# Kernel optimization log

Measured on AMD Instinct MI355X. Metric: run time of the kernel, lower is better.

Reference implementation:

```python
import jax, jax.numpy as jnp
import numpy as np

B, T, Z, AE, H, M, A = 32, 512, 128, 16, 1024, 5, 18
OUT = Z * 3 * M + 1  # 1921
K = M * Z  # per-component split size for logmix/mu/logstd


def setup_inputs() -> dict:
    key = jax.random.key(0)
    ks = jax.random.split(key, 9)
    s = 0.02
    return {
        "z": jax.random.normal(ks[0], (B, T, Z), jnp.float32),
        "actions": jax.random.randint(ks[1], (B, T), 0, A, jnp.int32),
        "dones": jax.random.randint(ks[2], (B, T), 0, 2, jnp.int32),
        "embed": jax.random.normal(ks[3], (A, AE), jnp.float32) * s,
        "W_ih": jax.random.normal(ks[4], (4 * H, Z + AE), jnp.float32) * s,
        "W_hh": jax.random.normal(ks[5], (4 * H, H), jnp.float32) * s,
        "b_ih": jnp.zeros((4 * H,), jnp.float32),
        "b_hh": jnp.zeros((4 * H,), jnp.float32),
        "W_out": jax.random.normal(ks[6], (OUT, H), jnp.float32) * s,
        "b_out": jnp.zeros((OUT,), jnp.float32),
    }


def reference(z, actions, dones, embed, W_ih, W_hh, b_ih, b_hh, W_out, b_out):
    a_emb = embed[actions]                              # [B,T,AE]
    inp = jnp.concatenate([z, a_emb], axis=2)           # [B,T,Z+AE]
    d = dones.astype(inp.dtype)                         # [B,T]
    # precompute input contribution to gates for all timesteps (one big GEMM)
    x_pre = jnp.einsum('btf,gf->btg', inp, W_ih) + b_ih + b_hh  # [B,T,4H]

    def cell(carry, xt):
        h, c = carry
        xg, dt = xt                                     # xg: [B,4H], dt: [B]
        gates = xg + h @ W_hh.T
        i, f, g, o = jnp.split(gates, 4, axis=1)        # torch LSTMCell order i,f,g,o
        c_new = jax.nn.sigmoid(f) * c + jax.nn.sigmoid(i) * jnp.tanh(g)
        h_new = jax.nn.sigmoid(o) * jnp.tanh(c_new)
        mask = (1.0 - dt)[:, None]                      # done-masking AFTER output
        return (h_new * mask, c_new * mask), h_new

    h0 = jnp.zeros((B, H), inp.dtype)
    _, hs = jax.lax.scan(cell, (h0, h0), (x_pre.transpose(1, 0, 2), d.T))
    hs = hs.transpose(1, 0, 2)[:, :-1]                  # [B,T-1,H]
    out = hs @ W_out.T + b_out                          # [B,T-1,OUT]

    logmix = out[..., :K].reshape(-1, M)
    mu = out[..., K:2 * K].reshape(-1, M)
    logstd = out[..., 2 * K:3 * K].reshape(-1, M)
    done_p = out[..., 3 * K:].squeeze(-1)               # [B,T-1]
    logmix = logmix - jax.scipy.special.logsumexp(logmix, axis=1, keepdims=True)
    return logmix, mu, logstd, done_p
```

## Files before the change

kernel.cpp:

```cpp
#include <hip/hip_runtime.h>
#include <hip/hip_bf16.h>


typedef float f4 __attribute__((ext_vector_type(4)));
typedef short s8 __attribute__((ext_vector_type(8)));
typedef unsigned short us8v __attribute__((ext_vector_type(8)));
typedef unsigned short us4v __attribute__((ext_vector_type(4)));
typedef unsigned long long u64;
typedef unsigned u32;

#define DEV __device__ __forceinline__

DEV unsigned short f2b(float f) {
  unsigned u = __float_as_uint(f);
  return (unsigned short)((u + 0x7FFFu + ((u >> 16) & 1u)) >> 16);
}
DEV float b2f(unsigned short s) { return __uint_as_float(((unsigned)s) << 16); }

DEV f4 MFMA(s8 a, s8 b, f4 c) {
  return __builtin_amdgcn_mfma_f32_16x16x32_bf16(a, b, c, 0, 0, 0);
}
DEV s8 LD8(const unsigned short* p) { return *reinterpret_cast<const s8*>(p); }

DEV u32 AL32(const u32* p) {
  return __hip_atomic_load(p, __ATOMIC_RELAXED, __HIP_MEMORY_SCOPE_AGENT);
}
DEV void AS(u64* p, u64 v) {
  __hip_atomic_store(p, v, __ATOMIC_RELAXED, __HIP_MEMORY_SCOPE_AGENT);
}

DEV float sigf(float x) {
  float e = __builtin_amdgcn_exp2f(x * -1.44269504f);
  return __builtin_amdgcn_rcpf(1.f + e);
}
DEV float tanhf_fast(float x) {
  float e = __builtin_amdgcn_exp2f(x * 2.88539008f);
  return 1.f - 2.f * __builtin_amdgcn_rcpf(e + 1.f);
}

static constexpr size_t WS_GCNT = 0;
static constexpr size_t WS_NACT = 2048;
static constexpr size_t WS_HDR  = 4096;
static constexpr size_t WS_META = 4352;
static constexpr size_t WS_LOFF = 69888;
static constexpr size_t WS_TMP  = 131072;
static constexpr size_t WS_ZT   = 131072;
static constexpr size_t WS_WOUT = 4325376;
static constexpr size_t WS_HS2  = 8261632;
static constexpr size_t WS_END  = 41816064;
static constexpr size_t DO_CALL = 35651584;

__global__ void cvt_wout_k(const float* __restrict__ W, unsigned short* __restrict__ o) {
  int i = blockIdx.x * 256 + threadIdx.x;
  if (i < 491776) {
    const float4 v = reinterpret_cast<const float4*>(W)[i];
    us4v u; u[0] = f2b(v.x); u[1] = f2b(v.y); u[2] = f2b(v.z); u[3] = f2b(v.w);
    reinterpret_cast<us4v*>(o)[i] = u;
  }
}

__global__ void cvt_z_k(const float* __restrict__ z, unsigned short* __restrict__ zt) {
  int i = blockIdx.x * 256 + threadIdx.x;
  if (i < 524288) {
    const float4 v = reinterpret_cast<const float4*>(z)[i];
    us4v u; u[0] = f2b(v.x); u[1] = f2b(v.y); u[2] = f2b(v.z); u[3] = f2b(v.w);
    reinterpret_cast<us4v*>(zt)[i] = u;
  }
}

__global__ void zero_hs_tail_k(u64* __restrict__ hs2) {
  int i = blockIdx.x * 256 + threadIdx.x;
  if (i < 8192) {
    int region = i >> 5, r = 16352 + (i & 31);
    hs2[(size_t)region * 16384 + r] = 0ull;
  }
}

__global__ __launch_bounds__(256) void seg_build_k(
    const int* __restrict__ dones, u32* __restrict__ tmp,
    u32* __restrict__ meta, u32* __restrict__ nact, u32* __restrict__ hdr,
    u32* __restrict__ loff) {
  __shared__ u32 hist[512];
  __shared__ u32 cur[512];
  __shared__ u32 scnt[32];
  const int tid = threadIdx.x;
  for (int i = tid; i < 512; i += 256) hist[i] = 0;
  __syncthreads();
  if (tid < 32) {
    int b = tid, cnt = 0, t0 = 0;
    for (int t = 1; t <= 511; ++t) {
      bool brk = (t == 511) || (dones[b * 512 + t - 1] != 0);
      if (brk) {
        int len = t - t0;
        tmp[b * 511 + cnt] = ((u32)t0 << 16) | (u32)len;
        atomicAdd(&hist[len], 1u);
        ++cnt; t0 = t;
      }
    }
    scnt[b] = (u32)cnt;
  }
  __syncthreads();
  if (tid == 0) {
    u32 acc = 0; int ml = 0;
    for (int L = 511; L >= 0; --L) {
      cur[L] = acc; nact[L] = acc;
      if (hist[L] && !ml) ml = L;
      acc += hist[L];
    }
    hdr[0] = acc; hdr[1] = (u32)ml;
    u32 off = 0; loff[0] = 0;
    for (int s2 = 1; s2 <= ml; ++s2) { loff[s2] = off; off += nact[s2]; }
  }
  __syncthreads();
  if (tid < 32) {
    int b = tid; u32 c = scnt[b];
    for (u32 i = 0; i < c; ++i) {
      u32 e = tmp[b * 511 + i];
      u32 len = e & 0xFFFFu, t0 = e >> 16;
      u32 slot = atomicAdd(&cur[len], 1u);
      meta[slot] = ((u32)b << 20) | (t0 << 10) | len;
    }
  }
}

__global__ __launch_bounds__(1024, 1) void lstm_seg_k(
    const float* __restrict__ Whh, const float* __restrict__ Wih,
    const float* __restrict__ embed, const float* __restrict__ bih,
    const float* __restrict__ bhh, const int* __restrict__ actions,
    const unsigned short* __restrict__ zt, const u32* __restrict__ meta,
    const u32* __restrict__ nact, const u32* __restrict__ hdr,
    const u32* __restrict__ loff, u64* __restrict__ hsl,
    u64* __restrict__ c_all, u64* __restrict__ hs2,
    u32* __restrict__ gcnt) {
  const int blk = blockIdx.x;
  const int tid = threadIdx.x;
  const int lane = tid & 63;
  const int w = tid >> 6;
  const int ln = lane & 15, lk = lane >> 4;
  const int slane = lane & 31;
  const int ehalf = lane >> 5;

  __shared__ alignas(16) unsigned short whh_sw[32 * 64 * 8];
  __shared__ alignas(16) unsigned short wz_sw[4 * 64 * 8];
  __shared__ float abias[18][16];
  __shared__ float red[16][32][17];

  for (int i = tid; i < 32 * 64 * 8; i += 1024) {
    int j = i & 7, L = (i >> 3) & 63, kt = i >> 9;
    int n = L & 15;
    int grow = (n >> 2) * 1024 + blk * 4 + (n & 3);
    int k = kt * 32 + ((L >> 4) << 3) + j;
    whh_sw[i] = f2b(Whh[grow * 1024 + k]);
  }
  for (int i = tid; i < 4 * 64 * 8; i += 1024) {
    int j = i & 7, L = (i >> 3) & 63, kt = i >> 9;
    int n = L & 15;
    int grow = (n >> 2) * 1024 + blk * 4 + (n & 3);
    int k = kt * 32 + ((L >> 4) << 3) + j;
    wz_sw[i] = f2b(Wih[grow * 144 + k]);
  }
  for (int i = tid; i < 18 * 16; i += 1024) {
    int a = i >> 4, n = i & 15;
    int grow = (n >> 2) * 1024 + blk * 4 + (n & 3);
    float s = bih[grow] + bhh[grow];
    for (int j = 0; j < 16; ++j) s += embed[a * 16 + j] * Wih[grow * 144 + 128 + j];
    abias[a][n] = s;
  }
  __syncthreads();

  const int maxlen = (int)hdr[1];

  for (int s = 0; s < maxlen; ++s) {
    const u32 N = nact[s];
    const int ntiles = (int)((N + 31) >> 5);
    const u64* hread = hsl + (size_t)loff[s] * 256;
    u64* hwrite = hsl + (size_t)loff[s + 1] * 256;

    for (int tile = w; tile < ntiles; tile += 16) {
      const u32 sb = (u32)tile << 5;
      const u32 slot = sb + (u32)slane;
      const bool valid = slot < N;
      const u32 m = valid ? meta[slot] : 0u;
      const u32 b = m >> 20, t0 = (m >> 10) & 1023u, L = m & 1023u;
      const int zrow = (int)(b * 512u + t0 + (u32)s);
      const int orow = (int)(b * 511u + t0 + (u32)s);
      const u32 act = valid ? (u32)actions[zrow] : 0u;
      u64 cq = 0;
      if (s && valid)
        cq = c_all[((size_t)blk << 14) + ((size_t)slot << 1) + ehalf];
      const int zr0 = __shfl(zrow, ln, 64);
      const int zr1 = __shfl(zrow, ln + 16, 64);

      f4 acc0 = {0.f, 0.f, 0.f, 0.f};
      f4 acc1 = {0.f, 0.f, 0.f, 0.f};
#pragma unroll
      for (int kz = 0; kz < 4; ++kz) {
        s8 a0 = LD8(zt + (size_t)zr0 * 128 + kz * 32 + (lk << 3));
        s8 a1 = LD8(zt + (size_t)zr1 * 128 + kz * 32 + (lk << 3));
        s8 bf = LD8(wz_sw + ((kz * 64 + lane) << 3));
        acc0 = MFMA(a0, bf, acc0);
        acc1 = MFMA(a1, bf, acc1);
      }
      if (s) {
        const u32 rA = sb + (u32)ln;
        const u32 rB = rA + 16u;
        const u32 rAc = (rA < N) ? rA : (N - 1u);
        const u32 rBc = (rB < N) ? rB : (N - 1u);
        const unsigned short* hrow0 =
            (const unsigned short*)(hread + (size_t)rAc * 256 + (lk << 1));
        const unsigned short* hrow1 =
            (const unsigned short*)(hread + (size_t)rBc * 256 + (lk << 1));
#pragma unroll 8
        for (int kt = 0; kt < 32; ++kt) {
          s8 fa = LD8(hrow0 + (kt << 5));
          s8 fb = LD8(hrow1 + (kt << 5));
          s8 bf = LD8(whh_sw + ((kt * 64 + lane) << 3));
          acc0 = MFMA(fa, bf, acc0);
          acc1 = MFMA(fb, bf, acc1);
        }
      }

#pragma unroll
      for (int j = 0; j < 4; ++j) {
        red[w][(lk << 2) + j][ln] = acc0[j];
        red[w][16 + (lk << 2) + j][ln] = acc1[j];
      }
      const bool carry = valid && (L > (u32)(s + 1));
      u32 hbits = 0;
      u32 cbits0 = 0, cbits1 = 0;
#pragma unroll
      for (int e = 0; e < 2; ++e) {
        const int eq = (ehalf << 1) + e;
        float gi = red[w][slane][eq]      + abias[act][eq];
        float gf = red[w][slane][4 + eq]  + abias[act][4 + eq];
        float gg = red[w][slane][8 + eq]  + abias[act][8 + eq];
        float go = red[w][slane][12 + eq] + abias[act][12 + eq];
        const float cprev = (e == 0) ? __uint_as_float((u32)cq)
                                     : __uint_as_float((u32)(cq >> 32));
        const float si = sigf(gi), sf = sigf(gf), so = sigf(go);
        const float cn = sf * cprev + si * tanhf_fast(gg);
        const float hn = so * tanhf_fast(cn);
        if (e == 0) cbits0 = __float_as_uint(cn); else cbits1 = __float_as_uint(cn);
        hbits |= ((u32)f2b(hn)) << (16 * e);
      }
      if (carry)
        c_all[((size_t)blk << 14) + ((size_t)slot << 1) + ehalf] =
            ((u64)cbits1 << 32) | (u64)cbits0;
      const u32 other = (u32)__shfl_xor((int)hbits, 32, 64);
      if (lane < 32 && valid) {
        const u64 hu = ((u64)other << 32) | (u64)hbits;
        hs2[((size_t)blk << 14) + orow] = hu;
        if (carry) AS(hwrite + (size_t)slot * 256 + blk, hu);
      }
    }

    asm volatile("s_waitcnt vmcnt(0)" ::: "memory");
    __syncthreads();
    if (s + 1 < maxlen) {
      if (tid == 0) {
        __hip_atomic_fetch_add(gcnt + (blk >> 4) * 32, 1u,
                               __ATOMIC_RELAXED, __HIP_MEMORY_SCOPE_AGENT);
        const u32 tgt = (u32)(s + 1) * 16u;
        for (u32 spin = 0; spin < (1u << 20); ++spin) {
          u32 mn = 0xFFFFFFFFu;
#pragma unroll
          for (int g = 0; g < 16; ++g) {
            u32 v = AL32(gcnt + g * 32);
            mn = (v < mn) ? v : mn;
          }
          if (mn >= tgt) break;
          __builtin_amdgcn_s_sleep(1);
        }
      }
      __syncthreads();
    }
  }
}

__global__ __launch_bounds__(256, 2) void out_gemm_k(
    const u64* __restrict__ hs2, const unsigned short* __restrict__ wout,
    const float* __restrict__ b_out, float* __restrict__ out) {
  const int mblk = blockIdx.x, nblk = blockIdx.y;
  const int tid = threadIdx.x, lane = tid & 63, w = tid >> 6;
  const int ln = lane & 15, lk = lane >> 4;
  __shared__ alignas(16) unsigned char smraw[21760];
  unsigned short* bsm = (unsigned short*)smraw;
  float* ep = (float*)smraw;

  const int r0 = mblk * 64 + w * 16;
  f4 acc[5];
#pragma unroll
  for (int s = 0; s < 5; ++s) acc[s] = (f4){0.f, 0.f, 0.f, 0.f};

  for (int kc = 0; kc < 8; ++kc) {
#pragma unroll
    for (int ii = 0; ii < 5; ++ii) {
      int i = tid + ii * 256;
      int n = i >> 4, k16 = i & 15;
      us8v v = *reinterpret_cast<const us8v*>(
          wout + (size_t)(nblk * 80 + n) * 1024 + kc * 128 + (k16 << 3));
      *reinterpret_cast<us8v*>(bsm + n * 136 + (k16 << 3)) = v;
    }
    __syncthreads();
#pragma unroll
    for (int ks = 0; ks < 4; ++ks) {
      const int k0 = kc * 128 + ks * 32 + (lk << 3);
      union { u64 q[2]; s8 v; } ua;
      ua.q[0] = hs2[(size_t)(k0 >> 2) * 16384 + r0 + ln];
      ua.q[1] = hs2[((size_t)(k0 >> 2) + 1) * 16384 + r0 + ln];
#pragma unroll
      for (int s = 0; s < 5; ++s) {
        s8 b = LD8(bsm + (s * 16 + ln) * 136 + ks * 32 + (lk << 3));
        acc[s] = MFMA(ua.v, b, acc[s]);
      }
    }
    __syncthreads();
  }

  const int T = nblk >> 3;
  if (T) {
    float* base = out + (size_t)10465280 * T;
    const int lc0 = (nblk - (T << 3)) * 80;
#pragma unroll
    for (int s = 0; s < 5; ++s) {
      const int lc = lc0 + s * 16 + ln;
      const float bias = b_out[T * 640 + lc];
#pragma unroll
      for (int j = 0; j < 4; ++j) {
        const int row = r0 + (lk << 2) + j;
        if (row < 16352) base[(size_t)row * 640 + lc] = acc[s][j] + bias;
      }
    }
  } else {
#pragma unroll
    for (int s = 0; s < 5; ++s) {
      const float bias = b_out[nblk * 80 + s * 16 + ln];
#pragma unroll
      for (int j = 0; j < 4; ++j)
        ep[(w * 16 + (lk << 2) + j) * 84 + s * 16 + ln] = acc[s][j] + bias;
    }
    __syncthreads();
    for (int task = tid; task < 1024; task += 256) {
      const int rr = task >> 4, grp = task & 15;
      const int row = mblk * 64 + rr;
      const float* e = ep + rr * 84 + grp * 5;
      float v0 = e[0], v1 = e[1], v2 = e[2], v3 = e[3], v4 = e[4];
      float mx = fmaxf(fmaxf(fmaxf(v0, v1), fmaxf(v2, v3)), v4);
      float ssum = expf(v0 - mx) + expf(v1 - mx) + expf(v2 - mx) +
                   expf(v3 - mx) + expf(v4 - mx);
      float lse = mx + logf(ssum);
      if (row < 16352) {
        float* o = out + (size_t)row * 640 + nblk * 80 + grp * 5;
        o[0] = v0 - lse; o[1] = v1 - lse; o[2] = v2 - lse;
        o[3] = v3 - lse; o[4] = v4 - lse;
      }
    }
  }
}

__global__ __launch_bounds__(256) void donep_k(
    const u64* __restrict__ hs2, const unsigned short* __restrict__ wout,
    const float* __restrict__ b_out, float* __restrict__ out) {
  const int lane = threadIdx.x & 63;
  const int wv = (blockIdx.x * 256 + threadIdx.x) >> 6;
  const unsigned short* wrow = wout + (size_t)1920 * 1024 + lane * 16;
  float wl[16];
#pragma unroll
  for (int i = 0; i < 16; ++i) wl[i] = b2f(wrow[i]);
  const float bias = b_out[1920];
  for (int r = wv; r < 16352; r += 2048) {
    float d = 0.f;
#pragma unroll
    for (int j = 0; j < 4; ++j) {
      union { u64 q; unsigned short h[4]; } u;
      u.q = hs2[(size_t)(lane * 4 + j) * 16384 + r];
#pragma unroll
      for (int i = 0; i < 4; ++i) d += b2f(u.h[i]) * wl[j * 4 + i];
    }
#pragma unroll
    for (int off = 32; off; off >>= 1) d += __shfl_down(d, off, 64);
    if (lane == 0) out[31395840 + r] = d + bias;
  }
}

extern "C" void kernel_launch(void* const* d_in, const int* in_sizes, int n_in,
                              void* d_out, int out_size, void* d_ws, size_t ws_size,
                              hipStream_t stream) {
  const float* z       = (const float*)d_in[0];
  const int*   actions = (const int*)d_in[1];
  const int*   dones   = (const int*)d_in[2];
  const float* embed   = (const float*)d_in[3];
  const float* Wih     = (const float*)d_in[4];
  const float* Whh     = (const float*)d_in[5];
  const float* bih     = (const float*)d_in[6];
  const float* bhh     = (const float*)d_in[7];
  const float* Wout    = (const float*)d_in[8];
  const float* bout    = (const float*)d_in[9];
  float* out = (float*)d_out;

  if (ws_size < WS_END) return;

  char* ws = (char*)d_ws;
  u32* gcnt              = (u32*)(ws + WS_GCNT);
  u32* nact              = (u32*)(ws + WS_NACT);
  u32* hdr               = (u32*)(ws + WS_HDR);
  u32* metaA             = (u32*)(ws + WS_META);
  u32* loff              = (u32*)(ws + WS_LOFF);
  u32* tmp               = (u32*)(ws + WS_TMP);
  unsigned short* zt     = (unsigned short*)(ws + WS_ZT);
  unsigned short* wout16 = (unsigned short*)(ws + WS_WOUT);
  u64* hs2               = (u64*)(ws + WS_HS2);
  u64* hsl   = (u64*)d_out;
  u64* call  = (u64*)((char*)d_out + DO_CALL);

  hipMemsetAsync(d_ws, 0, 2048, stream);

  seg_build_k<<<1, 256, 0, stream>>>(dones, tmp, metaA, nact, hdr, loff);
  cvt_z_k<<<2048, 256, 0, stream>>>(z, zt);
  zero_hs_tail_k<<<32, 256, 0, stream>>>(hs2);
  lstm_seg_k<<<256, 1024, 0, stream>>>(Whh, Wih, embed, bih, bhh, actions,
                                       zt, metaA, nact, hdr, loff, hsl, call,
                                       hs2, gcnt);
  cvt_wout_k<<<1921, 256, 0, stream>>>(Wout, wout16);
  out_gemm_k<<<dim3(256, 24), 256, 0, stream>>>(hs2, wout16, bout, out);
  donep_k<<<512, 256, 0, stream>>>(hs2, wout16, bout, out);
}
```

Baseline: 1.046 ms.

## Widen LSTM wave tiles to 64 rows and fuse done_p into output GEMM

```diff
diff --git a/kernel.cpp b/kernel.cpp
--- a/kernel.cpp
+++ b/kernel.cpp
@@ -137,13 +137,11 @@
   const int lane = tid & 63;
   const int w = tid >> 6;
   const int ln = lane & 15, lk = lane >> 4;
-  const int slane = lane & 31;
-  const int ehalf = lane >> 5;
 
   __shared__ alignas(16) unsigned short whh_sw[32 * 64 * 8];
   __shared__ alignas(16) unsigned short wz_sw[4 * 64 * 8];
   __shared__ float abias[18][16];
-  __shared__ float red[16][32][17];
+  __shared__ float red[16][64][17];
 
   for (int i = tid; i < 32 * 64 * 8; i += 1024) {
     int j = i & 7, L = (i >> 3) & 63, kt = i >> 9;
@@ -172,83 +170,97 @@
 
   for (int s = 0; s < maxlen; ++s) {
     const u32 N = nact[s];
-    const int ntiles = (int)((N + 31) >> 5);
+    const int ntiles = (int)((N + 63) >> 6);
     const u64* hread = hsl + (size_t)loff[s] * 256;
     u64* hwrite = hsl + (size_t)loff[s + 1] * 256;
 
     for (int tile = w; tile < ntiles; tile += 16) {
-      const u32 sb = (u32)tile << 5;
-      const u32 slot = sb + (u32)slane;
+      const u32 sb = (u32)tile << 6;
+      const u32 slot = sb + (u32)lane;
       const bool valid = slot < N;
       const u32 m = valid ? meta[slot] : 0u;
       const u32 b = m >> 20, t0 = (m >> 10) & 1023u, L = m & 1023u;
       const int zrow = (int)(b * 512u + t0 + (u32)s);
       const int orow = (int)(b * 511u + t0 + (u32)s);
       const u32 act = valid ? (u32)actions[zrow] : 0u;
-      u64 cq = 0;
-      if (s && valid)
-        cq = c_all[((size_t)blk << 14) + ((size_t)slot << 1) + ehalf];
-      const int zr0 = __shfl(zrow, ln, 64);
-      const int zr1 = __shfl(zrow, ln + 16, 64);
-
-      f4 acc0 = {0.f, 0.f, 0.f, 0.f};
-      f4 acc1 = {0.f, 0.f, 0.f, 0.f};
+      union { u64 q[2]; } cc; cc.q[0] = 0; cc.q[1] = 0;
+      if (s && valid) {
+        const u64* cp = c_all + ((size_t)blk << 14) + ((size_t)slot << 1);
+        cc.q[0] = cp[0]; cc.q[1] = cp[1];
+      }
+      int zr[4];
+#pragma unroll
+      for (int q = 0; q < 4; ++q) zr[q] = __shfl(zrow, ln + 16 * q, 64);
+
+      f4 acc0 = {0.f,0.f,0.f,0.f}, acc1 = {0.f,0.f,0.f,0.f};
+      f4 acc2 = {0.f,0.f,0.f,0.f}, acc3 = {0.f,0.f,0.f,0.f};
 #pragma unroll
       for (int kz = 0; kz < 4; ++kz) {
-        s8 a0 = LD8(zt + (size_t)zr0 * 128 + kz * 32 + (lk << 3));
-        s8 a1 = LD8(zt + (size_t)zr1 * 128 + kz * 32 + (lk << 3));
         s8 bf = LD8(wz_sw + ((kz * 64 + lane) << 3));
-        acc0 = MFMA(a0, bf, acc0);
-        acc1 = MFMA(a1, bf, acc1);
+        s8 a0 = LD8(zt + (size_t)zr[0] * 128 + kz * 32 + (lk << 3));
+        s8 a1 = LD8(zt + (size_t)zr[1] * 128 + kz * 32 + (lk << 3));
+        s8 a2 = LD8(zt + (size_t)zr[2] * 128 + kz * 32 + (lk << 3));
+        s8 a3 = LD8(zt + (size_t)zr[3] * 128 + kz * 32 + (lk << 3));
+        acc0 = MFMA(a0, bf, acc0);  acc1 = MFMA(a1, bf, acc1);
+        acc2 = MFMA(a2, bf, acc2);  acc3 = MFMA(a3, bf, acc3);
       }
       if (s) {
-        const u32 rA = sb + (u32)ln;
-        const u32 rB = rA + 16u;
-        const u32 rAc = (rA < N) ? rA : (N - 1u);
-        const u32 rBc = (rB < N) ? rB : (N - 1u);
-        const unsigned short* hrow0 =
-            (const unsigned short*)(hread + (size_t)rAc * 256 + (lk << 1));
-        const unsigned short* hrow1 =
-            (const unsigned short*)(hread + (size_t)rBc * 256 + (lk << 1));
+        const u32 r0c = (sb + (u32)ln      < N) ? sb + (u32)ln      : N - 1u;
+        const u32 r1c = (sb + (u32)ln + 16 < N) ? sb + (u32)ln + 16 : N - 1u;
+        const u32 r2c = (sb + (u32)ln + 32 < N) ? sb + (u32)ln + 32 : N - 1u;
+        const u32 r3c = (sb + (u32)ln + 48 < N) ? sb + (u32)ln + 48 : N - 1u;
+        const unsigned short* h0 =
+            (const unsigned short*)(hread + (size_t)r0c * 256) + (lk << 3);
+        const unsigned short* h1 =
+            (const unsigned short*)(hread + (size_t)r1c * 256) + (lk << 3);
+        const unsigned short* h2 =
+            (const unsigned short*)(hread + (size_t)r2c * 256) + (lk << 3);
+        const unsigned short* h3 =
+            (const unsigned short*)(hread + (size_t)r3c * 256) + (lk << 3);
 #pragma unroll 8
         for (int kt = 0; kt < 32; ++kt) {
-          s8 fa = LD8(hrow0 + (kt << 5));
-          s8 fb = LD8(hrow1 + (kt << 5));
           s8 bf = LD8(whh_sw + ((kt * 64 + lane) << 3));
-          acc0 = MFMA(fa, bf, acc0);
-          acc1 = MFMA(fb, bf, acc1);
+          s8 f0 = LD8(h0 + (kt << 5));
+          s8 f1 = LD8(h1 + (kt << 5));
+          s8 f2 = LD8(h2 + (kt << 5));
+          s8 f3 = LD8(h3 + (kt << 5));
+          acc0 = MFMA(f0, bf, acc0);  acc1 = MFMA(f1, bf, acc1);
+          acc2 = MFMA(f2, bf, acc2);  acc3 = MFMA(f3, bf, acc3);
         }
       }
 
 #pragma unroll
       for (int j = 0; j < 4; ++j) {
-        red[w][(lk << 2) + j][ln] = acc0[j];
+        red[w][(lk << 2) + j][ln]      = acc0[j];
         red[w][16 + (lk << 2) + j][ln] = acc1[j];
+        red[w][32 + (lk << 2) + j][ln] = acc2[j];
+        red[w][48 + (lk << 2) + j][ln] = acc3[j];
       }
       const bool carry = valid && (L > (u32)(s + 1));
-      u32 hbits = 0;
-      u32 cbits0 = 0, cbits1 = 0;
-#pragma unroll
-      for (int e = 0; e < 2; ++e) {
-        const int eq = (ehalf << 1) + e;
-        float gi = red[w][slane][eq]      + abias[act][eq];
-        float gf = red[w][slane][4 + eq]  + abias[act][4 + eq];
-        float gg = red[w][slane][8 + eq]  + abias[act][8 + eq];
-        float go = red[w][slane][12 + eq] + abias[act][12 + eq];
-        const float cprev = (e == 0) ? __uint_as_float((u32)cq)
-                                     : __uint_as_float((u32)(cq >> 32));
+      u32 cb[4]; unsigned short hb[4];
+#pragma unroll
+      for (int e = 0; e < 4; ++e) {
+        float gi = red[w][lane][e]      + abias[act][e];
+        float gf = red[w][lane][4 + e]  + abias[act][4 + e];
+        float gg = red[w][lane][8 + e]  + abias[act][8 + e];
+        float go = red[w][lane][12 + e] + abias[act][12 + e];
+        const u32 cpb = (e == 0) ? (u32)cc.q[0] : (e == 1) ? (u32)(cc.q[0] >> 32)
+                       : (e == 2) ? (u32)cc.q[1] : (u32)(cc.q[1] >> 32);
+        const float cprev = __uint_as_float(cpb);
         const float si = sigf(gi), sf = sigf(gf), so = sigf(go);
         const float cn = sf * cprev + si * tanhf_fast(gg);
         const float hn = so * tanhf_fast(cn);
-        if (e == 0) cbits0 = __float_as_uint(cn); else cbits1 = __float_as_uint(cn);
-        hbits |= ((u32)f2b(hn)) << (16 * e);
-      }
-      if (carry)
-        c_all[((size_t)blk << 14) + ((size_t)slot << 1) + ehalf] =
-            ((u64)cbits1 << 32) | (u64)cbits0;
-      const u32 other = (u32)__shfl_xor((int)hbits, 32, 64);
-      if (lane < 32 && valid) {
-        const u64 hu = ((u64)other << 32) | (u64)hbits;
+        cb[e] = __float_as_uint(cn);
+        hb[e] = f2b(hn);
+      }
+      if (carry) {
+        u64* cp = c_all + ((size_t)blk << 14) + ((size_t)slot << 1);
+        cp[0] = ((u64)cb[1] << 32) | (u64)cb[0];
+        cp[1] = ((u64)cb[3] << 32) | (u64)cb[2];
+      }
+      const u64 hu = (u64)hb[0] | ((u64)hb[1] << 16) |
+                     ((u64)hb[2] << 32) | ((u64)hb[3] << 48);
+      if (valid) {
         hs2[((size_t)blk << 14) + orow] = hu;
         if (carry) AS(hwrite + (size_t)slot * 256 + blk, hu);
       }
@@ -283,14 +295,21 @@
   const int mblk = blockIdx.x, nblk = blockIdx.y;
   const int tid = threadIdx.x, lane = tid & 63, w = tid >> 6;
   const int ln = lane & 15, lk = lane >> 4;
-  __shared__ alignas(16) unsigned char smraw[21760];
+  __shared__ alignas(16) unsigned char smraw[26112];
   unsigned short* bsm = (unsigned short*)smraw;
   float* ep = (float*)smraw;
+  const bool last = (nblk == 23);
+
+  if (last) {
+    for (int i = tid; i < 15 * 136; i += 256) bsm[81 * 136 + i] = 0;
+  }
+  __syncthreads();
 
   const int r0 = mblk * 64 + w * 16;
   f4 acc[5];
 #pragma unroll
   for (int s = 0; s < 5; ++s) acc[s] = (f4){0.f, 0.f, 0.f, 0.f};
+  f4 acc5 = {0.f, 0.f, 0.f, 0.f};
 
   for (int kc = 0; kc < 8; ++kc) {
 #pragma unroll
@@ -301,6 +320,11 @@
           wout + (size_t)(nblk * 80 + n) * 1024 + kc * 128 + (k16 << 3));
       *reinterpret_cast<us8v*>(bsm + n * 136 + (k16 << 3)) = v;
     }
+    if (last && tid < 16) {
+      us8v v = *reinterpret_cast<const us8v*>(
+          wout + (size_t)1920 * 1024 + kc * 128 + (tid << 3));
+      *reinterpret_cast<us8v*>(bsm + 80 * 136 + (tid << 3)) = v;
+    }
     __syncthreads();
 #pragma unroll
     for (int ks = 0; ks < 4; ++ks) {
@@ -313,6 +337,10 @@
         s8 b = LD8(bsm + (s * 16 + ln) * 136 + ks * 32 + (lk << 3));
         acc[s] = MFMA(ua.v, b, acc[s]);
       }
+      if (last) {
+        s8 b6 = LD8(bsm + ((80 + ln) * 136) + ks * 32 + (lk << 3));
+        acc5 = MFMA(ua.v, b6, acc5);
+      }
     }
     __syncthreads();
   }
@@ -329,6 +357,14 @@
       for (int j = 0; j < 4; ++j) {
         const int row = r0 + (lk << 2) + j;
         if (row < 16352) base[(size_t)row * 640 + lc] = acc[s][j] + bias;
+      }
+    }
+    if (last && ln == 0) {
+      const float bias = b_out[1920];
+#pragma unroll
+      for (int j = 0; j < 4; ++j) {
+        const int row = r0 + (lk << 2) + j;
+        if (row < 16352) out[31395840 + row] = acc5[j] + bias;
       }
     }
   } else {
@@ -358,31 +394,6 @@
   }
 }
 
-__global__ __launch_bounds__(256) void donep_k(
-    const u64* __restrict__ hs2, const unsigned short* __restrict__ wout,
-    const float* __restrict__ b_out, float* __restrict__ out) {
-  const int lane = threadIdx.x & 63;
-  const int wv = (blockIdx.x * 256 + threadIdx.x) >> 6;
-  const unsigned short* wrow = wout + (size_t)1920 * 1024 + lane * 16;
-  float wl[16];
-#pragma unroll
-  for (int i = 0; i < 16; ++i) wl[i] = b2f(wrow[i]);
-  const float bias = b_out[1920];
-  for (int r = wv; r < 16352; r += 2048) {
-    float d = 0.f;
-#pragma unroll
-    for (int j = 0; j < 4; ++j) {
-      union { u64 q; unsigned short h[4]; } u;
-      u.q = hs2[(size_t)(lane * 4 + j) * 16384 + r];
-#pragma unroll
-      for (int i = 0; i < 4; ++i) d += b2f(u.h[i]) * wl[j * 4 + i];
-    }
-#pragma unroll
-    for (int off = 32; off; off >>= 1) d += __shfl_down(d, off, 64);
-    if (lane == 0) out[31395840 + r] = d + bias;
-  }
-}
-
 extern "C" void kernel_launch(void* const* d_in, const int* in_sizes, int n_in,
                               void* d_out, int out_size, void* d_ws, size_t ws_size,
                               hipStream_t stream) {
@@ -423,5 +434,4 @@
                                        hs2, gcnt);
   cvt_wout_k<<<1921, 256, 0, stream>>>(Wout, wout16);
   out_gemm_k<<<dim3(256, 24), 256, 0, stream>>>(hs2, wout16, bout, out);
-  donep_k<<<512, 256, 0, stream>>>(hs2, wout16, bout, out);
-}
+}
```

After: 1.036 ms. Within noise of the previous version (-0.9%).
